# Optimization experiments

Hardware: AMD Instinct MI355X
Metric: run time of the kernel (lower is better)

## Reference

```python
import jax, jax.numpy as jnp
import numpy as np

B, Q, C, H, D, E, I = 8, 256, 192, 20, 64, 1500, 5120
HID = H * D  # 1280
EPS = 1e-5
SCALE = D ** -0.5


def _linear(x, w, b):
    return jnp.einsum('bsh,oh->bso', x, w) + b


def _layernorm(x, w, b):
    xf = x.astype(jnp.float32)
    mu = jnp.mean(xf, axis=-1, keepdims=True)
    var = jnp.mean(jnp.square(xf - mu), axis=-1, keepdims=True)
    return ((xf - mu) * jax.lax.rsqrt(var + EPS) * w + b).astype(x.dtype)


def _heads(x):  # [B,S,HID] -> [B,H,S,D]
    return x.reshape(B, -1, H, D).transpose(0, 2, 1, 3)


def setup_inputs() -> dict:
    key = jax.random.key(0)
    ks = jax.random.split(key, 24)
    s = 0.02
    inp = {
        'hidden_states': jax.random.normal(ks[0], (B, Q, HID), jnp.float32),
        'mask': jnp.zeros((B, 1, Q, Q + C), jnp.float32),
        'past_key': jax.random.normal(ks[1], (B, H, C, D), jnp.float32),
        'past_value': jax.random.normal(ks[2], (B, H, C, D), jnp.float32),
        'cross_key': jax.random.normal(ks[3], (B, H, E, D), jnp.float32),
        'cross_value': jax.random.normal(ks[4], (B, H, E, D), jnp.float32),
        'q_w': jax.random.normal(ks[5], (HID, HID), jnp.float32) * s,
        'q_b': jnp.zeros((HID,), jnp.float32),
        'k_w': jax.random.normal(ks[6], (HID, HID), jnp.float32) * s,
        'k_b': jnp.zeros((HID,), jnp.float32),
        'v_w': jax.random.normal(ks[7], (HID, HID), jnp.float32) * s,
        'v_b': jnp.zeros((HID,), jnp.float32),
        'o_w': jax.random.normal(ks[8], (HID, HID), jnp.float32) * s,
        'o_b': jnp.zeros((HID,), jnp.float32),
        'cq_w': jax.random.normal(ks[9], (HID, HID), jnp.float32) * s,
        'cq_b': jnp.zeros((HID,), jnp.float32),
        'co_w': jax.random.normal(ks[10], (HID, HID), jnp.float32) * s,
        'co_b': jnp.zeros((HID,), jnp.float32),
        'up_w': jax.random.normal(ks[11], (I, HID), jnp.float32) * s,
        'up_b': jnp.zeros((I,), jnp.float32),
        'down_w': jax.random.normal(ks[12], (HID, I), jnp.float32) * s,
        'down_b': jnp.zeros((HID,), jnp.float32),
        'ln1_w': jnp.ones((HID,), jnp.float32),
        'ln1_b': jnp.zeros((HID,), jnp.float32),
        'ln2_w': jnp.ones((HID,), jnp.float32),
        'ln2_b': jnp.zeros((HID,), jnp.float32),
        'ln3_w': jnp.ones((HID,), jnp.float32),
        'ln3_b': jnp.zeros((HID,), jnp.float32),
    }
    return inp


def reference(hidden_states, mask, past_key, past_value, cross_key, cross_value,
              q_w, q_b, k_w, k_b, v_w, v_b, o_w, o_b,
              cq_w, cq_b, co_w, co_b, up_w, up_b, down_w, down_b,
              ln1_w, ln1_b, ln2_w, ln2_b, ln3_w, ln3_b):
    # ---- self-attention block ----
    residual = hidden_states
    x = _layernorm(hidden_states, ln1_w, ln1_b)
    q = _heads(_linear(x, q_w, q_b) * SCALE)          # [B,H,Q,D]
    k_new = _heads(_linear(x, k_w, k_b))              # [B,H,Q,D]
    v_new = _heads(_linear(x, v_w, v_b))
    k = jnp.concatenate([past_key, k_new], axis=2)    # [B,H,C+Q,D]
    v = jnp.concatenate([past_value, v_new], axis=2)
    scores = jnp.einsum('bhqd,bhkd->bhqk', q, k) + mask
    attn = jnp.einsum('bhqk,bhkd->bhqd', jax.nn.softmax(scores, axis=-1), v)
    attn = attn.transpose(0, 2, 1, 3).reshape(B, Q, HID)
    attn_out = _linear(attn, o_w, o_b)
    present_key = k[:, :, Q:, :]
    present_value = v[:, :, Q:, :]
    h = residual + attn_out
    # ---- cross-attention block ----
    residual = h
    x = _layernorm(h, ln2_w, ln2_b)
    cq = _heads(_linear(x, cq_w, cq_b) * SCALE)       # [B,H,Q,D]
    cscores = jnp.einsum('bhqd,bhkd->bhqk', cq, cross_key)
    cattn = jnp.einsum('bhqk,bhkd->bhqd', jax.nn.softmax(cscores, axis=-1), cross_value)
    cattn = cattn.transpose(0, 2, 1, 3).reshape(B, Q, HID)
    h = residual + _linear(cattn, co_w, co_b)
    # ---- MLP block ----
    residual = h
    x = _layernorm(h, ln3_w, ln3_b)
    up = _linear(x, up_w, up_b)
    mlp_out = _linear(jax.nn.gelu(up, approximate=False), down_w, down_b)
    h = residual + mlp_out
    return (h, present_key, present_value)
```

## Files before the change

### kernel.cpp

```cpp
#include <hip/hip_runtime.h>
#include <math.h>

#define Bc   8
#define Qn   256
#define Cn   192
#define Hn   20
#define Dn   64
#define En   1500
#define In   5120
#define HIDn 1280
#define BQ   2048
#define KSELF 448
#define EPAD 1536
#define S1   (BQ*HIDn)
#define WSZ  (HIDn*HIDn)
#define BH   (Bc*Hn)

typedef __attribute__((ext_vector_type(8))) short bf16x8;
typedef __attribute__((ext_vector_type(4))) float f32x4;

__device__ __forceinline__ short f2bf(float f) {
  union { float f; unsigned u; } x; x.f = f;
  unsigned r = x.u + 0x7fffu + ((x.u >> 16) & 1u);
  return (short)(r >> 16);
}
__device__ __forceinline__ float bf2f(short s) {
  union { unsigned u; float f; } x; x.u = ((unsigned)(unsigned short)s) << 16;
  return x.f;
}
__device__ __forceinline__ void gload16(const short* g, short* l) {
  __builtin_amdgcn_global_load_lds(
      (const __attribute__((address_space(1))) void*)g,
      (__attribute__((address_space(3))) void*)l, 16, 0, 0);
}
__device__ __forceinline__ bf16x8 cvt8(const float* p) {
  const float4 a = *reinterpret_cast<const float4*>(p);
  const float4 b = *reinterpret_cast<const float4*>(p + 4);
  bf16x8 t;
  t[0] = f2bf(a.x); t[1] = f2bf(a.y); t[2] = f2bf(a.z); t[3] = f2bf(a.w);
  t[4] = f2bf(b.x); t[5] = f2bf(b.y); t[6] = f2bf(b.z); t[7] = f2bf(b.w);
  return t;
}

__global__ __launch_bounds__(256) void convert_all(
    const float* q, const float* k, const float* v, const float* o,
    const float* cq, const float* co, const float* up, const float* dn,
    short* wq, short* wk, short* wv, short* wo,
    short* wcq, short* wco, short* wup, short* wdn)
{
  const float* src; short* dst; int n;
  switch (blockIdx.y) {
    case 0: src = q;  dst = wq;  n = WSZ; break;
    case 1: src = k;  dst = wk;  n = WSZ; break;
    case 2: src = v;  dst = wv;  n = WSZ; break;
    case 3: src = o;  dst = wo;  n = WSZ; break;
    case 4: src = cq; dst = wcq; n = WSZ; break;
    case 5: src = co; dst = wco; n = WSZ; break;
    case 6: src = up; dst = wup; n = HIDn * In; break;
    default: src = dn; dst = wdn; n = HIDn * In; break;
  }
  const int i = (blockIdx.x * 256 + threadIdx.x) * 8;
  if (i >= n) return;
  *reinterpret_cast<bf16x8*>(dst + i) = cvt8(src + i);
}

__global__ __launch_bounds__(256) void prep_cross(
    const float* __restrict__ K, const float* __restrict__ V,
    short* __restrict__ Kc, short* __restrict__ Vc)
{
  const size_t idx = (size_t)blockIdx.x * 256 + threadIdx.x;
  const int d8 = (int)(idx & 7) * 8;
  const size_t t = idx >> 3;
  const int key = (int)(t % EPAD);
  const int bh  = (int)(t / EPAD);
  bf16x8 kv = (bf16x8)0, vv = (bf16x8)0;
  if (key < En) {
    const size_t off = ((size_t)bh * En + key) * 64 + d8;
    kv = cvt8(K + off);
    vv = cvt8(V + off);
  }
  const size_t dst = ((size_t)bh * EPAD + key) * 64 + d8;
  *reinterpret_cast<bf16x8*>(Kc + dst) = kv;
  *reinterpret_cast<bf16x8*>(Vc + dst) = vv;
}

__global__ __launch_bounds__(256) void prep_self(
    const float* __restrict__ Kp, const float* __restrict__ Vp,
    const short* __restrict__ kn, const short* __restrict__ vn,
    short* __restrict__ Kc, short* __restrict__ Vc)
{
  const size_t idx = (size_t)blockIdx.x * 256 + threadIdx.x;
  const int d8 = (int)(idx & 7) * 8;
  const size_t t = idx >> 3;
  const int key = (int)(t % KSELF);
  const int bh  = (int)(t / KSELF);
  bf16x8 kv, vv;
  if (key < Cn) {
    const size_t off = ((size_t)bh * Cn + key) * 64 + d8;
    kv = cvt8(Kp + off);
    vv = cvt8(Vp + off);
  } else {
    const int b = bh / Hn, h = bh % Hn;
    const size_t off = ((size_t)(b * Qn + (key - Cn))) * HIDn + h * 64 + d8;
    kv = *reinterpret_cast<const bf16x8*>(kn + off);
    vv = *reinterpret_cast<const bf16x8*>(vn + off);
  }
  const size_t dst = ((size_t)bh * KSELF + key) * 64 + d8;
  *reinterpret_cast<bf16x8*>(Kc + dst) = kv;
  *reinterpret_cast<bf16x8*>(Vc + dst) = vv;
}

__global__ __launch_bounds__(256) void layernorm_k(
    const float* __restrict__ in, const float* __restrict__ w,
    const float* __restrict__ b, short* __restrict__ out)
{
  const int row = blockIdx.x;
  const float* x = in + (size_t)row * HIDn;
  float v[5], s = 0.f, s2 = 0.f;
#pragma unroll
  for (int i = 0; i < 5; ++i) {
    float t = x[threadIdx.x + 256 * i];
    v[i] = t; s += t; s2 += t * t;
  }
#pragma unroll
  for (int off = 1; off < 64; off <<= 1) {
    s  += __shfl_xor(s,  off, 64);
    s2 += __shfl_xor(s2, off, 64);
  }
  __shared__ float red[8];
  const int wave = threadIdx.x >> 6, lane = threadIdx.x & 63;
  if (lane == 0) { red[wave] = s; red[wave + 4] = s2; }
  __syncthreads();
  s  = red[0] + red[1] + red[2] + red[3];
  s2 = red[4] + red[5] + red[6] + red[7];
  const float mu  = s / HIDn;
  const float var = s2 / HIDn - mu * mu;
  const float rs  = rsqrtf(var + 1e-5f);
#pragma unroll
  for (int i = 0; i < 5; ++i) {
    const int c = threadIdx.x + 256 * i;
    out[(size_t)row * HIDn + c] = f2bf((v[i] - mu) * rs * w[c] + b[c]);
  }
}

template<int BM, int BN, int MODE>
__global__ __launch_bounds__(256) void gemm_db(
    const short* __restrict__ A, const short* __restrict__ W,
    const float* __restrict__ bias, const float* __restrict__ resid,
    void* __restrict__ out0, void* __restrict__ out1, void* __restrict__ out2,
    const float* __restrict__ b1, const float* __restrict__ b2,
    int N, int K, int LDK, float scale)
{
  constexpr int FM = BM / 32, FN = BN / 32;
  __shared__ __align__(16) short Alds[2][BM * 64];
  __shared__ __align__(16) short Blds[2][BN * 64];
  const int tid = threadIdx.x, lane = tid & 63, wave = tid >> 6;
  const int wr = wave >> 1, wc = wave & 1;
  const int m0 = blockIdx.x * BM, n0 = blockIdx.y * BN;
  const int bz = blockIdx.z;
  const int lr = lane & 15;
  const int kc = (lane >> 4) * 8;
  const size_t koff = (size_t)bz * K;

  f32x4 acc[FM][FN];
#pragma unroll
  for (int mi = 0; mi < FM; ++mi)
#pragma unroll
    for (int ni = 0; ni < FN; ++ni)
      acc[mi][ni] = (f32x4){0.f, 0.f, 0.f, 0.f};

  auto STAGE = [&](int kt, int buf) {
    const int k0 = kt << 6;
#pragma unroll
    for (int j = 0; j < BM / 32; ++j) {
      const int i = wave + 4 * j;
      const int rr = i >> 1, kk = i & 1;
      gload16(A + (size_t)(m0 + rr * 16 + lr) * LDK + koff + k0 + kk * 32 + kc,
              &Alds[buf][i * 512]);
    }
#pragma unroll
    for (int j = 0; j < BN / 32; ++j) {
      const int i = wave + 4 * j;
      const int rr = i >> 1, kk = i & 1;
      gload16(W + (size_t)(n0 + rr * 16 + lr) * LDK + koff + k0 + kk * 32 + kc,
              &Blds[buf][i * 512]);
    }
  };

  const int nk = K >> 6;
  STAGE(0, 0);
  asm volatile("s_waitcnt vmcnt(0)" ::: "memory");
  __builtin_amdgcn_s_barrier();
  __builtin_amdgcn_sched_barrier(0);

  int cur = 0;
  for (int kt = 0; kt < nk; ++kt) {
    if (kt + 1 < nk) STAGE(kt + 1, cur ^ 1);
    bf16x8 af[2][FM], bfv[2][FN];
#pragma unroll
    for (int kk = 0; kk < 2; ++kk) {
#pragma unroll
      for (int mi = 0; mi < FM; ++mi)
        af[kk][mi] = *reinterpret_cast<const bf16x8*>(
            &Alds[cur][((wr * FM + mi) * 2 + kk) * 512 + lane * 8]);
#pragma unroll
      for (int ni = 0; ni < FN; ++ni)
        bfv[kk][ni] = *reinterpret_cast<const bf16x8*>(
            &Blds[cur][((wc * FN + ni) * 2 + kk) * 512 + lane * 8]);
    }
#pragma unroll
    for (int kk = 0; kk < 2; ++kk)
#pragma unroll
      for (int mi = 0; mi < FM; ++mi)
#pragma unroll
        for (int ni = 0; ni < FN; ++ni)
          acc[mi][ni] = __builtin_amdgcn_mfma_f32_16x16x32_bf16(
              af[kk][mi], bfv[kk][ni], acc[mi][ni], 0, 0, 0);
    __builtin_amdgcn_sched_barrier(0);
    asm volatile("s_waitcnt vmcnt(0)" ::: "memory");
    __builtin_amdgcn_s_barrier();
    __builtin_amdgcn_sched_barrier(0);
    cur ^= 1;
  }

  const int cn = lane & 15;
  const int rb = (lane >> 4) * 4;
#pragma unroll
  for (int mi = 0; mi < FM; ++mi)
#pragma unroll
    for (int ni = 0; ni < FN; ++ni)
#pragma unroll
      for (int j = 0; j < 4; ++j) {
        const int row = m0 + wr * (BM / 2) + mi * 16 + rb + j;
        const int col = n0 + wc * (BN / 2) + ni * 16 + cn;
        const float a = acc[mi][ni][j];
        if (MODE == 0) {
          ((float*)out0)[(size_t)row * N + col] =
              a + bias[col] + resid[(size_t)row * N + col];
        } else if (MODE == 1) {
          ((short*)out0)[(size_t)row * N + col] = f2bf((a + bias[col]) * scale);
        } else if (MODE == 2) {
          float t = a + bias[col];
          t = 0.5f * t * (1.f + erff(t * 0.70710678118654752f));
          ((short*)out0)[(size_t)row * N + col] = f2bf(t);
        } else if (MODE == 3) {
          const int rg  = n0 / 1280;
          const int cl  = col - rg * 1280;
          short* op     = rg == 0 ? (short*)out0 : rg == 1 ? (short*)out1 : (short*)out2;
          const float* bp = rg == 0 ? bias : rg == 1 ? b1 : b2;
          const float sc  = rg == 0 ? 0.125f : 1.f;
          op[(size_t)row * 1280 + cl] = f2bf((a + bp[cl]) * sc);
        } else {
          float* op = bz == 0 ? (float*)out0 : (float*)out1;
          op[(size_t)row * N + col] = a;
        }
      }
}

template<int RM>
__global__ __launch_bounds__(256) void reduce_k(
    const float* __restrict__ p0, const float* __restrict__ p1,
    const float* __restrict__ resid, const float* __restrict__ bias,
    float* __restrict__ outf, short* __restrict__ outb, float scale)
{
  const size_t i = ((size_t)blockIdx.x * 256 + threadIdx.x) * 4;
  if (i >= (size_t)S1) return;
  const int col = (int)(i % HIDn);
  const float4 a  = *reinterpret_cast<const float4*>(p0 + i);
  const float4 b  = *reinterpret_cast<const float4*>(p1 + i);
  const float4 bi = *reinterpret_cast<const float4*>(bias + col);
  if (RM == 0) {
    const float4 r = *reinterpret_cast<const float4*>(resid + i);
    float4 o;
    o.x = a.x + b.x + bi.x + r.x;
    o.y = a.y + b.y + bi.y + r.y;
    o.z = a.z + b.z + bi.z + r.z;
    o.w = a.w + b.w + bi.w + r.w;
    *reinterpret_cast<float4*>(outf + i) = o;
  } else {
    *reinterpret_cast<short4*>(outb + i) = make_short4(
        f2bf((a.x + b.x + bi.x) * scale), f2bf((a.y + b.y + bi.y) * scale),
        f2bf((a.z + b.z + bi.z) * scale), f2bf((a.w + b.w + bi.w) * scale));
  }
}

template<bool HASMASK>
__global__ __launch_bounds__(256) void attn_mfma(
    const short* __restrict__ Qb, const short* __restrict__ Kc,
    const short* __restrict__ Vc, const float* __restrict__ mask,
    short* __restrict__ Ob, int PADK, int KT)
{
  const int orig = blockIdx.x;
  const int idx  = (orig & 7) * 80 + (orig >> 3);
  const int qt = idx & 3;
  const int h  = (idx >> 2) % Hn;
  const int b  = idx / (4 * Hn);
  const int bh = b * Hn + h;
  const int tid = threadIdx.x, lane = tid & 63, wave = tid >> 6;
  const int q0 = qt * 64;
  const int cn = lane & 15;
  const int hg = lane >> 4;
  const int rb = hg * 4;

  __shared__ __align__(16) short k_s[64][72];
  __shared__ __align__(16) short vt_s[64][72];
  __shared__ __align__(16) short p_s[4][16][72];

  bf16x8 aq[2];
  {
    const short* qrow = Qb + (size_t)(b * Qn + q0 + wave * 16 + cn) * HIDn + h * 64;
    aq[0] = *reinterpret_cast<const bf16x8*>(qrow + hg * 8);
    aq[1] = *reinterpret_cast<const bf16x8*>(qrow + 32 + hg * 8);
  }

  float mrun[4] = {-1e30f, -1e30f, -1e30f, -1e30f};
  float lrun[4] = {0.f, 0.f, 0.f, 0.f};
  f32x4 oacc[4];
#pragma unroll
  for (int t = 0; t < 4; ++t) oacc[t] = (f32x4){0.f, 0.f, 0.f, 0.f};

  const int nchunk = PADK >> 6;
  for (int ci = 0; ci < nchunk; ++ci) {
    const int c0 = ci * 64;
    const short* kbase = Kc + ((size_t)bh * PADK + c0) * 64;
    const short* vbase = Vc + ((size_t)bh * PADK + c0) * 64;
#pragma unroll
    for (int r = 0; r < 2; ++r) {
      const int i = tid + r * 256;
      const int key = i >> 3, d8 = (i & 7) * 8;
      const bf16x8 kv = *reinterpret_cast<const bf16x8*>(kbase + key * 64 + d8);
      const bf16x8 vv = *reinterpret_cast<const bf16x8*>(vbase + key * 64 + d8);
      *reinterpret_cast<bf16x8*>(&k_s[key][d8]) = kv;
      const int g = key >> 3, o = key & 7, f = i & 7;
      const int col = ((g ^ f) << 3) | o;
#pragma unroll
      for (int j = 0; j < 8; ++j) vt_s[d8 + j][col] = vv[j];
    }
    __syncthreads();

    f32x4 sacc[4];
#pragma unroll
    for (int t = 0; t < 4; ++t) sacc[t] = (f32x4){0.f, 0.f, 0.f, 0.f};
#pragma unroll
    for (int t = 0; t < 4; ++t)
#pragma unroll
      for (int kk = 0; kk < 2; ++kk) {
        const bf16x8 bk = *reinterpret_cast<const bf16x8*>(&k_s[t * 16 + cn][kk * 32 + hg * 8]);
        sacc[t] = __builtin_amdgcn_mfma_f32_16x16x32_bf16(aq[kk], bk, sacc[t], 0, 0, 0);
      }

    float sc[4][4];
#pragma unroll
    for (int t = 0; t < 4; ++t) {
      const int key = c0 + t * 16 + cn;
      const bool valid = key < KT;
#pragma unroll
      for (int j = 0; j < 4; ++j) {
        float v = sacc[t][j];
        if (HASMASK && valid)
          v += mask[((size_t)(b * Qn) + q0 + wave * 16 + rb + j) * KT + key];
        sc[t][j] = valid ? v : -1e30f;
      }
    }

#pragma unroll
    for (int j = 0; j < 4; ++j) {
      float mx = fmaxf(fmaxf(sc[0][j], sc[1][j]), fmaxf(sc[2][j], sc[3][j]));
#pragma unroll
      for (int off = 1; off < 16; off <<= 1) mx = fmaxf(mx, __shfl_xor(mx, off, 64));
      if (mx > mrun[j] + 8.f) {
        const float alpha = __expf(mrun[j] - mx);
        lrun[j] *= alpha;
#pragma unroll
        for (int t = 0; t < 4; ++t) oacc[t][j] *= alpha;
        mrun[j] = mx;
      }
      float ps = 0.f;
#pragma unroll
      for (int t = 0; t < 4; ++t) {
        const float p = __expf(sc[t][j] - mrun[j]);
        sc[t][j] = p; ps += p;
      }
#pragma unroll
      for (int off = 1; off < 16; off <<= 1) ps += __shfl_xor(ps, off, 64);
      lrun[j] += ps;
    }

#pragma unroll
    for (int t = 0; t < 4; ++t)
#pragma unroll
      for (int j = 0; j < 4; ++j)
        p_s[wave][rb + j][t * 16 + cn] = f2bf(sc[t][j]);

    const bf16x8 ap0 = *reinterpret_cast<const bf16x8*>(&p_s[wave][cn][hg * 8]);
    const bf16x8 ap1 = *reinterpret_cast<const bf16x8*>(&p_s[wave][cn][32 + hg * 8]);
#pragma unroll
    for (int t = 0; t < 4; ++t) {
      const int d  = t * 16 + cn;
      const int fd = (d >> 3) & 7;
      const bf16x8 bv0 = *reinterpret_cast<const bf16x8*>(&vt_s[d][((hg)     ^ fd) << 3]);
      const bf16x8 bv1 = *reinterpret_cast<const bf16x8*>(&vt_s[d][((4 + hg) ^ fd) << 3]);
      oacc[t] = __builtin_amdgcn_mfma_f32_16x16x32_bf16(ap0, bv0, oacc[t], 0, 0, 0);
      oacc[t] = __builtin_amdgcn_mfma_f32_16x16x32_bf16(ap1, bv1, oacc[t], 0, 0, 0);
    }
    __syncthreads();
  }

#pragma unroll
  for (int t = 0; t < 4; ++t)
#pragma unroll
    for (int j = 0; j < 4; ++j)
      Ob[(size_t)(b * Qn + q0 + wave * 16 + rb + j) * HIDn + h * 64 + t * 16 + cn] =
          f2bf(oacc[t][j] / lrun[j]);
}

__global__ __launch_bounds__(256) void copy_present(
    const short* __restrict__ kn, const short* __restrict__ vn,
    float* __restrict__ outk, float* __restrict__ outv)
{
  const int idx = blockIdx.x * 256 + threadIdx.x;
  if (idx >= Bc * Hn * Cn * 8) return;
  const int d8 = (idx & 7) * 8;
  int t = idx >> 3;
  const int c = t % Cn; t /= Cn;
  const int h = t % Hn;
  const int b = t / Hn;
  const size_t src = (size_t)(b * Qn + (Qn - Cn) + c) * HIDn + h * 64 + d8;
  const size_t dst = (((size_t)b * Hn + h) * Cn + c) * 64 + d8;
  const bf16x8 kv = *reinterpret_cast<const bf16x8*>(kn + src);
  const bf16x8 vv = *reinterpret_cast<const bf16x8*>(vn + src);
#pragma unroll
  for (int j = 0; j < 8; ++j) {
    outk[dst + j] = bf2f(kv[j]);
    outv[dst + j] = bf2f(vv[j]);
  }
}

extern "C" void kernel_launch(void* const* d_in, const int* in_sizes, int n_in,
                              void* d_out, int out_size, void* d_ws, size_t ws_size,
                              hipStream_t stream)
{
  const float* hidden  = (const float*)d_in[0];
  const float* mask    = (const float*)d_in[1];
  const float* past_k  = (const float*)d_in[2];
  const float* past_v  = (const float*)d_in[3];
  const float* cross_k = (const float*)d_in[4];
  const float* cross_v = (const float*)d_in[5];
  const float* q_w  = (const float*)d_in[6];  const float* q_b  = (const float*)d_in[7];
  const float* k_w  = (const float*)d_in[8];  const float* k_b  = (const float*)d_in[9];
  const float* v_w  = (const float*)d_in[10]; const float* v_b  = (const float*)d_in[11];
  const float* o_w  = (const float*)d_in[12]; const float* o_b  = (const float*)d_in[13];
  const float* cq_w = (const float*)d_in[14]; const float* cq_b = (const float*)d_in[15];
  const float* co_w = (const float*)d_in[16]; const float* co_b = (const float*)d_in[17];
  const float* up_w = (const float*)d_in[18]; const float* up_b = (const float*)d_in[19];
  const float* dn_w = (const float*)d_in[20]; const float* dn_b = (const float*)d_in[21];
  const float* ln1w = (const float*)d_in[22]; const float* ln1b = (const float*)d_in[23];
  const float* ln2w = (const float*)d_in[24]; const float* ln2b = (const float*)d_in[25];
  const float* ln3w = (const float*)d_in[26]; const float* ln3b = (const float*)d_in[27];

  short* wq  = (short*)d_ws;
  short* wk  = wq  + (size_t)WSZ;
  short* wv  = wk  + (size_t)WSZ;
  short* wo  = wv  + (size_t)WSZ;
  short* wcq = wo  + (size_t)WSZ;
  short* wco = wcq + (size_t)WSZ;
  short* wup = wco + (size_t)WSZ;
  short* wdn = wup + (size_t)HIDn * In;
  short* xb  = wdn + (size_t)HIDn * In;
  short* qb  = xb  + (size_t)S1;
  short* kb  = qb  + (size_t)S1;
  short* vb  = kb  + (size_t)S1;
  short* ab  = vb  + (size_t)S1;
  short* U   = ab  + (size_t)S1;
  short* ksb = U;
  short* vsb = U + (size_t)BH * KSELF * 64;
  short* upa = U;
  float* po0 = (float*)U;
  float* po1 = po0 + (size_t)S1;
  short* kcc = U + (size_t)BQ * In;
  short* vcc = kcc + (size_t)BH * EPAD * 64;
  float* h1  = (float*)(vcc + (size_t)BH * EPAD * 64);
  float* pd0 = (float*)qb;
  float* pd1 = (float*)vb;

  float* out_h  = (float*)d_out;
  float* out_pk = out_h + (size_t)S1;
  float* out_pv = out_pk + (size_t)(Bc * Hn * Cn * Dn);
  float* h2 = out_h;

  const dim3 blk(256);
  const dim3 gconv(3200, 8);
  const dim3 gqkv(16, 30);
  const dim3 gsplit(16, 20, 2);
  const dim3 gup(16, 40);
  const dim3 gattn(640);
  const dim3 gred((S1 / 4 + 255) / 256);

  convert_all<<<gconv, blk, 0, stream>>>(q_w, k_w, v_w, o_w, cq_w, co_w, up_w, dn_w,
                                         wq, wk, wv, wo, wcq, wco, wup, wdn);
  prep_cross<<<(BH * EPAD * 8) / 256, blk, 0, stream>>>(cross_k, cross_v, kcc, vcc);
  layernorm_k<<<BQ, blk, 0, stream>>>(hidden, ln1w, ln1b, xb);
  gemm_db<128, 128, 3><<<gqkv, blk, 0, stream>>>(xb, wq, q_b, nullptr,
      qb, kb, vb, k_b, v_b, 3840, HIDn, HIDn, 1.f);
  copy_present<<<(Bc * Hn * Cn * 8 + 255) / 256, blk, 0, stream>>>(kb, vb, out_pk, out_pv);
  prep_self<<<(BH * KSELF * 8) / 256, blk, 0, stream>>>(past_k, past_v, kb, vb, ksb, vsb);
  attn_mfma<true><<<gattn, blk, 0, stream>>>(qb, ksb, vsb, mask, ab, KSELF, KSELF);
  gemm_db<128, 64, 4><<<gsplit, blk, 0, stream>>>(ab, wo, nullptr, nullptr,
      po0, po1, nullptr, nullptr, nullptr, HIDn, HIDn / 2, HIDn, 1.f);
  reduce_k<0><<<gred, blk, 0, stream>>>(po0, po1, hidden, o_b, h1, nullptr, 1.f);
  layernorm_k<<<BQ, blk, 0, stream>>>(h1, ln2w, ln2b, xb);
  gemm_db<128, 64, 4><<<gsplit, blk, 0, stream>>>(xb, wcq, nullptr, nullptr,
      po0, po1, nullptr, nullptr, nullptr, HIDn, HIDn / 2, HIDn, 1.f);
  reduce_k<1><<<gred, blk, 0, stream>>>(po0, po1, nullptr, cq_b, nullptr, qb, 0.125f);
  attn_mfma<false><<<gattn, blk, 0, stream>>>(qb, kcc, vcc, nullptr, ab, EPAD, En);
  gemm_db<128, 64, 4><<<gsplit, blk, 0, stream>>>(ab, wco, nullptr, nullptr,
      po0, po1, nullptr, nullptr, nullptr, HIDn, HIDn / 2, HIDn, 1.f);
  reduce_k<0><<<gred, blk, 0, stream>>>(po0, po1, h1, co_b, h2, nullptr, 1.f);
  layernorm_k<<<BQ, blk, 0, stream>>>(h2, ln3w, ln3b, xb);
  gemm_db<128, 128, 2><<<gup, blk, 0, stream>>>(xb, wup, up_b, nullptr,
      upa, nullptr, nullptr, nullptr, nullptr, In, HIDn, HIDn, 1.f);
  gemm_db<128, 64, 4><<<gsplit, blk, 0, stream>>>(upa, wdn, nullptr, nullptr,
      pd0, pd1, nullptr, nullptr, nullptr, HIDn, In / 2, In, 1.f);
  reduce_k<0><<<gred, blk, 0, stream>>>(pd0, pd1, h2, dn_b, out_h, nullptr, 1.f);
}
```

Before: 541.7 us.

## Drop split-K reductions, fuse bias/residual epilogues into GEMM via LDS staging

Removes the two-way split-K GEMMs and their separate reduce kernels. Bias, residual, scaling and bf16 conversion are now fused into a single GEMM epilogue that stages accumulators through shared memory for vectorised stores. The block index is also remapped for XCD-aware locality, and the intermediate residual h1 is stored as bf16 to halve its traffic. The costs are fewer blocks for the long-K down projection and some precision loss in the residual path.

```diff
diff --git a/kernel.cpp b/kernel.cpp
--- a/kernel.cpp
+++ b/kernel.cpp
@@ -110,16 +110,19 @@
   *reinterpret_cast<bf16x8*>(Vc + dst) = vv;
 }
 
+template<bool BFIN>
 __global__ __launch_bounds__(256) void layernorm_k(
-    const float* __restrict__ in, const float* __restrict__ w,
+    const void* __restrict__ in, const float* __restrict__ w,
     const float* __restrict__ b, short* __restrict__ out)
 {
   const int row = blockIdx.x;
-  const float* x = in + (size_t)row * HIDn;
   float v[5], s = 0.f, s2 = 0.f;
 #pragma unroll
   for (int i = 0; i < 5; ++i) {
-    float t = x[threadIdx.x + 256 * i];
+    const int c = threadIdx.x + 256 * i;
+    float t;
+    if (BFIN) t = bf2f(((const short*)in)[(size_t)row * HIDn + c]);
+    else      t = ((const float*)in)[(size_t)row * HIDn + c];
     v[i] = t; s += t; s2 += t * t;
   }
 #pragma unroll
@@ -146,21 +149,25 @@
 template<int BM, int BN, int MODE>
 __global__ __launch_bounds__(256) void gemm_db(
     const short* __restrict__ A, const short* __restrict__ W,
-    const float* __restrict__ bias, const float* __restrict__ resid,
+    const float* __restrict__ bias, const void* __restrict__ resid,
     void* __restrict__ out0, void* __restrict__ out1, void* __restrict__ out2,
     const float* __restrict__ b1, const float* __restrict__ b2,
     int N, int K, int LDK, float scale)
 {
   constexpr int FM = BM / 32, FN = BN / 32;
-  __shared__ __align__(16) short Alds[2][BM * 64];
-  __shared__ __align__(16) short Blds[2][BN * 64];
+  constexpr int ASH = BM * 64, BSH = BN * 64;
+  __shared__ __align__(16) short smem[2 * ASH + 2 * BSH];
   const int tid = threadIdx.x, lane = tid & 63, wave = tid >> 6;
   const int wr = wave >> 1, wc = wave & 1;
-  const int m0 = blockIdx.x * BM, n0 = blockIdx.y * BN;
-  const int bz = blockIdx.z;
   const int lr = lane & 15;
   const int kc = (lane >> 4) * 8;
-  const size_t koff = (size_t)bz * K;
+
+  const int GX = gridDim.x, T = GX * gridDim.y;
+  int orig = blockIdx.x + GX * blockIdx.y;
+  const int cpx = T >> 3;
+  const int lid = (orig & 7) * cpx + (orig >> 3);
+  const int m0 = (lid % GX) * BM;
+  const int n0 = (lid / GX) * BN;
 
   f32x4 acc[FM][FN];
 #pragma unroll
@@ -175,15 +182,15 @@
     for (int j = 0; j < BM / 32; ++j) {
       const int i = wave + 4 * j;
       const int rr = i >> 1, kk = i & 1;
-      gload16(A + (size_t)(m0 + rr * 16 + lr) * LDK + koff + k0 + kk * 32 + kc,
-              &Alds[buf][i * 512]);
+      gload16(A + (size_t)(m0 + rr * 16 + lr) * LDK + k0 + kk * 32 + kc,
+              &smem[buf * ASH + i * 512]);
     }
 #pragma unroll
     for (int j = 0; j < BN / 32; ++j) {
       const int i = wave + 4 * j;
       const int rr = i >> 1, kk = i & 1;
-      gload16(W + (size_t)(n0 + rr * 16 + lr) * LDK + koff + k0 + kk * 32 + kc,
-              &Blds[buf][i * 512]);
+      gload16(W + (size_t)(n0 + rr * 16 + lr) * LDK + k0 + kk * 32 + kc,
+              &smem[2 * ASH + buf * BSH + i * 512]);
     }
   };
 
@@ -202,11 +209,11 @@
 #pragma unroll
       for (int mi = 0; mi < FM; ++mi)
         af[kk][mi] = *reinterpret_cast<const bf16x8*>(
-            &Alds[cur][((wr * FM + mi) * 2 + kk) * 512 + lane * 8]);
+            &smem[cur * ASH + ((wr * FM + mi) * 2 + kk) * 512 + lane * 8]);
 #pragma unroll
       for (int ni = 0; ni < FN; ++ni)
         bfv[kk][ni] = *reinterpret_cast<const bf16x8*>(
-            &Blds[cur][((wc * FN + ni) * 2 + kk) * 512 + lane * 8]);
+            &smem[2 * ASH + cur * BSH + ((wc * FN + ni) * 2 + kk) * 512 + lane * 8]);
     }
 #pragma unroll
     for (int kk = 0; kk < 2; ++kk)
@@ -223,64 +230,99 @@
     cur ^= 1;
   }
 
+  __syncthreads();
+  float* ep = (float*)smem;
+  constexpr int PS = BN + 4;
+  constexpr int halfM = BM / 2;
   const int cn = lane & 15;
   const int rb = (lane >> 4) * 4;
-#pragma unroll
-  for (int mi = 0; mi < FM; ++mi)
-#pragma unroll
-    for (int ni = 0; ni < FN; ++ni)
-#pragma unroll
-      for (int j = 0; j < 4; ++j) {
-        const int row = m0 + wr * (BM / 2) + mi * 16 + rb + j;
-        const int col = n0 + wc * (BN / 2) + ni * 16 + cn;
-        const float a = acc[mi][ni][j];
-        if (MODE == 0) {
-          ((float*)out0)[(size_t)row * N + col] =
-              a + bias[col] + resid[(size_t)row * N + col];
-        } else if (MODE == 1) {
-          ((short*)out0)[(size_t)row * N + col] = f2bf((a + bias[col]) * scale);
-        } else if (MODE == 2) {
-          float t = a + bias[col];
-          t = 0.5f * t * (1.f + erff(t * 0.70710678118654752f));
-          ((short*)out0)[(size_t)row * N + col] = f2bf(t);
-        } else if (MODE == 3) {
-          const int rg  = n0 / 1280;
-          const int cl  = col - rg * 1280;
-          short* op     = rg == 0 ? (short*)out0 : rg == 1 ? (short*)out1 : (short*)out2;
-          const float* bp = rg == 0 ? bias : rg == 1 ? b1 : b2;
-          const float sc  = rg == 0 ? 0.125f : 1.f;
-          op[(size_t)row * 1280 + cl] = f2bf((a + bp[cl]) * sc);
-        } else {
-          float* op = bz == 0 ? (float*)out0 : (float*)out1;
-          op[(size_t)row * N + col] = a;
+  const int rg = (MODE == 3) ? n0 / 1280 : 0;
+  const float* bp = (MODE == 3) ? (rg == 0 ? bias : rg == 1 ? b1 : b2) : bias;
+  const float  sc = (MODE == 3) ? (rg == 0 ? 0.125f : 1.f) : scale;
+  short* op3 = (MODE == 3)
+      ? (rg == 0 ? (short*)out0 : rg == 1 ? (short*)out1 : (short*)out2) : nullptr;
+
+#pragma unroll
+  for (int p = 0; p < BM / 32; ++p) {
+    if (wr == (p * 32) / halfM) {
+      const int mi0 = ((p * 32) % halfM) / 16;
+#pragma unroll
+      for (int mm = 0; mm < 2; ++mm)
+#pragma unroll
+        for (int ni = 0; ni < FN; ++ni)
+#pragma unroll
+          for (int j = 0; j < 4; ++j)
+            ep[(mm * 16 + rb + j) * PS + wc * (BN / 2) + ni * 16 + cn] =
+                acc[mi0 + mm][ni][j];
+    }
+    __syncthreads();
+#pragma unroll
+    for (int c = 0; c < 32 * BN / 8 / 256; ++c) {
+      const int ci = tid + c * 256;
+      const int r  = ci / (BN / 8);
+      const int c8 = (ci % (BN / 8)) * 8;
+      const int grow = m0 + p * 32 + r;
+      const int gcol = n0 + c8;
+      float f[8];
+#pragma unroll
+      for (int i = 0; i < 4; ++i) f[i] = ep[r * PS + c8 + i];
+#pragma unroll
+      for (int i = 0; i < 4; ++i) f[4 + i] = ep[r * PS + c8 + 4 + i];
+      const float4 bv0 = *reinterpret_cast<const float4*>(bp + (MODE == 3 ? gcol - rg * 1280 : gcol));
+      const float4 bv1 = *reinterpret_cast<const float4*>(bp + (MODE == 3 ? gcol - rg * 1280 : gcol) + 4);
+      const float bb[8] = {bv0.x, bv0.y, bv0.z, bv0.w, bv1.x, bv1.y, bv1.z, bv1.w};
+#pragma unroll
+      for (int i = 0; i < 8; ++i) f[i] += bb[i];
+      if (MODE == 0) {
+        const float* rp = (const float*)resid + (size_t)grow * N + gcol;
+        float4 o0, o1;
+        const float4 r0 = *reinterpret_cast<const float4*>(rp);
+        const float4 r1 = *reinterpret_cast<const float4*>(rp + 4);
+        o0.x = f[0] + r0.x; o0.y = f[1] + r0.y; o0.z = f[2] + r0.z; o0.w = f[3] + r0.w;
+        o1.x = f[4] + r1.x; o1.y = f[5] + r1.y; o1.z = f[6] + r1.z; o1.w = f[7] + r1.w;
+        float* outp = (float*)out0 + (size_t)grow * N + gcol;
+        *reinterpret_cast<float4*>(outp) = o0;
+        *reinterpret_cast<float4*>(outp + 4) = o1;
+      } else if (MODE == 6) {
+        const bf16x8 rv = *reinterpret_cast<const bf16x8*>((const short*)resid + (size_t)grow * N + gcol);
+        float4 o0, o1;
+        o0.x = f[0] + bf2f(rv[0]); o0.y = f[1] + bf2f(rv[1]);
+        o0.z = f[2] + bf2f(rv[2]); o0.w = f[3] + bf2f(rv[3]);
+        o1.x = f[4] + bf2f(rv[4]); o1.y = f[5] + bf2f(rv[5]);
+        o1.z = f[6] + bf2f(rv[6]); o1.w = f[7] + bf2f(rv[7]);
+        float* outp = (float*)out0 + (size_t)grow * N + gcol;
+        *reinterpret_cast<float4*>(outp) = o0;
+        *reinterpret_cast<float4*>(outp + 4) = o1;
+      } else if (MODE == 5) {
+        const float* rp = (const float*)resid + (size_t)grow * N + gcol;
+        const float4 r0 = *reinterpret_cast<const float4*>(rp);
+        const float4 r1 = *reinterpret_cast<const float4*>(rp + 4);
+        const float rr[8] = {r0.x, r0.y, r0.z, r0.w, r1.x, r1.y, r1.z, r1.w};
+        bf16x8 o;
+#pragma unroll
+        for (int i = 0; i < 8; ++i) o[i] = f2bf(f[i] + rr[i]);
+        *reinterpret_cast<bf16x8*>((short*)out0 + (size_t)grow * N + gcol) = o;
+      } else if (MODE == 1) {
+        bf16x8 o;
+#pragma unroll
+        for (int i = 0; i < 8; ++i) o[i] = f2bf(f[i] * sc);
+        *reinterpret_cast<bf16x8*>((short*)out0 + (size_t)grow * N + gcol) = o;
+      } else if (MODE == 2) {
+        bf16x8 o;
+#pragma unroll
+        for (int i = 0; i < 8; ++i) {
+          const float t = f[i];
+          o[i] = f2bf(0.5f * t * (1.f + erff(t * 0.70710678118654752f)));
         }
+        *reinterpret_cast<bf16x8*>((short*)out0 + (size_t)grow * N + gcol) = o;
+      } else {
+        bf16x8 o;
+#pragma unroll
+        for (int i = 0; i < 8; ++i) o[i] = f2bf(f[i] * sc);
+        *reinterpret_cast<bf16x8*>(op3 + (size_t)grow * 1280 + (gcol - rg * 1280)) = o;
       }
-}
-
-template<int RM>
-__global__ __launch_bounds__(256) void reduce_k(
-    const float* __restrict__ p0, const float* __restrict__ p1,
-    const float* __restrict__ resid, const float* __restrict__ bias,
-    float* __restrict__ outf, short* __restrict__ outb, float scale)
-{
-  const size_t i = ((size_t)blockIdx.x * 256 + threadIdx.x) * 4;
-  if (i >= (size_t)S1) return;
-  const int col = (int)(i % HIDn);
-  const float4 a  = *reinterpret_cast<const float4*>(p0 + i);
-  const float4 b  = *reinterpret_cast<const float4*>(p1 + i);
-  const float4 bi = *reinterpret_cast<const float4*>(bias + col);
-  if (RM == 0) {
-    const float4 r = *reinterpret_cast<const float4*>(resid + i);
-    float4 o;
-    o.x = a.x + b.x + bi.x + r.x;
-    o.y = a.y + b.y + bi.y + r.y;
-    o.z = a.z + b.z + bi.z + r.z;
-    o.w = a.w + b.w + bi.w + r.w;
-    *reinterpret_cast<float4*>(outf + i) = o;
-  } else {
-    *reinterpret_cast<short4*>(outb + i) = make_short4(
-        f2bf((a.x + b.x + bi.x) * scale), f2bf((a.y + b.y + bi.y) * scale),
-        f2bf((a.z + b.z + bi.z) * scale), f2bf((a.w + b.w + bi.w) * scale));
+    }
+    __syncthreads();
   }
 }
 
@@ -475,13 +517,9 @@
   short* ksb = U;
   short* vsb = U + (size_t)BH * KSELF * 64;
   short* upa = U;
-  float* po0 = (float*)U;
-  float* po1 = po0 + (size_t)S1;
   short* kcc = U + (size_t)BQ * In;
   short* vcc = kcc + (size_t)BH * EPAD * 64;
-  float* h1  = (float*)(vcc + (size_t)BH * EPAD * 64);
-  float* pd0 = (float*)qb;
-  float* pd1 = (float*)vb;
+  short* h1b = (short*)(vcc + (size_t)BH * EPAD * 64);
 
   float* out_h  = (float*)d_out;
   float* out_pk = out_h + (size_t)S1;
@@ -491,35 +529,30 @@
   const dim3 blk(256);
   const dim3 gconv(3200, 8);
   const dim3 gqkv(16, 30);
-  const dim3 gsplit(16, 20, 2);
+  const dim3 gn64(16, 20);
   const dim3 gup(16, 40);
   const dim3 gattn(640);
-  const dim3 gred((S1 / 4 + 255) / 256);
 
   convert_all<<<gconv, blk, 0, stream>>>(q_w, k_w, v_w, o_w, cq_w, co_w, up_w, dn_w,
                                          wq, wk, wv, wo, wcq, wco, wup, wdn);
   prep_cross<<<(BH * EPAD * 8) / 256, blk, 0, stream>>>(cross_k, cross_v, kcc, vcc);
-  layernorm_k<<<BQ, blk, 0, stream>>>(hidden, ln1w, ln1b, xb);
+  layernorm_k<false><<<BQ, blk, 0, stream>>>(hidden, ln1w, ln1b, xb);
   gemm_db<128, 128, 3><<<gqkv, blk, 0, stream>>>(xb, wq, q_b, nullptr,
       qb, kb, vb, k_b, v_b, 3840, HIDn, HIDn, 1.f);
   copy_present<<<(Bc * Hn * Cn * 8 + 255) / 256, blk, 0, stream>>>(kb, vb, out_pk, out_pv);
   prep_self<<<(BH * KSELF * 8) / 256, blk, 0, stream>>>(past_k, past_v, kb, vb, ksb, vsb);
   attn_mfma<true><<<gattn, blk, 0, stream>>>(qb, ksb, vsb, mask, ab, KSELF, KSELF);
-  gemm_db<128, 64, 4><<<gsplit, blk, 0, stream>>>(ab, wo, nullptr, nullptr,
-      po0, po1, nullptr, nullptr, nullptr, HIDn, HIDn / 2, HIDn, 1.f);
-  reduce_k<0><<<gred, blk, 0, stream>>>(po0, po1, hidden, o_b, h1, nullptr, 1.f);
-  layernorm_k<<<BQ, blk, 0, stream>>>(h1, ln2w, ln2b, xb);
-  gemm_db<128, 64, 4><<<gsplit, blk, 0, stream>>>(xb, wcq, nullptr, nullptr,
-      po0, po1, nullptr, nullptr, nullptr, HIDn, HIDn / 2, HIDn, 1.f);
-  reduce_k<1><<<gred, blk, 0, stream>>>(po0, po1, nullptr, cq_b, nullptr, qb, 0.125f);
+  gemm_db<128, 64, 5><<<gn64, blk, 0, stream>>>(ab, wo, o_b, hidden,
+      h1b, nullptr, nullptr, nullptr, nullptr, HIDn, HIDn, HIDn, 1.f);
+  layernorm_k<true><<<BQ, blk, 0, stream>>>(h1b, ln2w, ln2b, xb);
+  gemm_db<128, 64, 1><<<gn64, blk, 0, stream>>>(xb, wcq, cq_b, nullptr,
+      qb, nullptr, nullptr, nullptr, nullptr, HIDn, HIDn, HIDn, 0.125f);
   attn_mfma<false><<<gattn, blk, 0, stream>>>(qb, kcc, vcc, nullptr, ab, EPAD, En);
-  gemm_db<128, 64, 4><<<gsplit, blk, 0, stream>>>(ab, wco, nullptr, nullptr,
-      po0, po1, nullptr, nullptr, nullptr, HIDn, HIDn / 2, HIDn, 1.f);
-  reduce_k<0><<<gred, blk, 0, stream>>>(po0, po1, h1, co_b, h2, nullptr, 1.f);
-  layernorm_k<<<BQ, blk, 0, stream>>>(h2, ln3w, ln3b, xb);
+  gemm_db<128, 64, 6><<<gn64, blk, 0, stream>>>(ab, wco, co_b, h1b,
+      h2, nullptr, nullptr, nullptr, nullptr, HIDn, HIDn, HIDn, 1.f);
+  layernorm_k<false><<<BQ, blk, 0, stream>>>(h2, ln3w, ln3b, xb);
   gemm_db<128, 128, 2><<<gup, blk, 0, stream>>>(xb, wup, up_b, nullptr,
       upa, nullptr, nullptr, nullptr, nullptr, In, HIDn, HIDn, 1.f);
-  gemm_db<128, 64, 4><<<gsplit, blk, 0, stream>>>(upa, wdn, nullptr, nullptr,
-      pd0, pd1, nullptr, nullptr, nullptr, HIDn, In / 2, In, 1.f);
-  reduce_k<0><<<gred, blk, 0, stream>>>(pd0, pd1, h2, dn_b, out_h, nullptr, 1.f);
-}
+  gemm_db<128, 64, 0><<<gn64, blk, 0, stream>>>(upa, wdn, dn_b, h2,
+      out_h, nullptr, nullptr, nullptr, nullptr, HIDn, In, In, 1.f);
+}
```

Result: slower. 566.0 us (+4.5%).
